# Kernel optimization log

Measured on AMD Instinct MI355X. Metric: run time of the kernel, lower is better.

The kernel has to match this reference:

```python
import jax
jax.config.update("jax_enable_x64", True)  # Sinkhorn runs in f64, matching torch's d.double()
import jax.numpy as jnp
import numpy as np

N, D, K = 32768, 128, 1024
TAU = 0.2
SK_EPS = 0.005
SK_ITERS = 3


def setup_inputs() -> dict:
    key = jax.random.key(0)
    k1, k2 = jax.random.split(key)
    x = jax.random.normal(k1, (N, D), dtype=jnp.float32)
    codebook = jax.random.normal(k2, (K, D), dtype=jnp.float32) * 0.02  # embedding.weight
    return {"x": x, "codebook": codebook}


def _l2norm(v):
    # F.normalize with eps=1e-12
    n = jnp.linalg.norm(v, axis=-1, keepdims=True)
    return v / jnp.maximum(n, 1e-12)


def _center_distance(d):
    d = jnp.where(jnp.isnan(d), jnp.zeros_like(d), d)
    mx, mn = d.max(), d.min()
    middle = (mx + mn) / 2
    amplitude = jnp.maximum(mx - middle + 1e-5, 1e-5)
    return (d - middle) / amplitude


def _sinkhorn(d, epsilon, iters):
    # d: [N, K] in f64; Q: [K, N]
    Q = jnp.exp(-d / epsilon).T
    Kc, B = Q.shape
    Q = Q / jnp.maximum(Q.sum(), 1e-5)

    def body(Q, _):
        Q = Q / Q.sum(axis=1, keepdims=True) / Kc
        Q = Q / Q.sum(axis=0, keepdims=True) / B
        return Q, None

    Q, _ = jax.lax.scan(body, Q, None, length=iters)
    return (Q * B).T  # [N, K]


def reference(x, codebook):
    latent = x.reshape(-1, codebook.shape[-1])  # [N, D]
    cos_sim = _l2norm(latent) @ _l2norm(codebook).T  # [N, K]
    d = (1.0 - cos_sim) / TAU

    # training path with sk_epsilon > 0: center + Sinkhorn (no_grad in torch)
    dc = _center_distance(jax.lax.stop_gradient(d))
    Q = _sinkhorn(dc.astype(jnp.float64), SK_EPS, SK_ITERS)
    indices = jnp.argmax(Q, axis=-1)  # [N]

    x_q = codebook[indices].reshape(x.shape)

    # cross-entropy(cos_sim / tau, indices.detach())
    logits = cos_sim / TAU
    logp = jax.nn.log_softmax(logits, axis=-1)
    loss = -jnp.mean(jnp.take_along_axis(logp, indices[:, None], axis=-1))

    # straight-through estimator
    x_q = x + jax.lax.stop_gradient(x_q - x)
    return x_q, loss, indices
```

## Files before the change

kernel.cpp:

```cpp
#include <hip/hip_runtime.h>
#include <cstddef>

#define NPTS 32768
#define DDIM 128
#define KCB  1024

typedef __attribute__((ext_vector_type(8))) short short8;
typedef __attribute__((ext_vector_type(4))) float f32x4;


__device__ __forceinline__ float hw_exp2(float x) {
#if __has_builtin(__builtin_amdgcn_exp2f)
  return __builtin_amdgcn_exp2f(x);
#else
  return exp2f(x);
#endif
}

__device__ __forceinline__ void atomic_add_f64(double* p, double v) {
  __hip_atomic_fetch_add(p, v, __ATOMIC_RELAXED, __HIP_MEMORY_SCOPE_AGENT);
}

__device__ __forceinline__ unsigned short bf16_rne(float v) {
  unsigned u = __float_as_uint(v);
  unsigned r = u + 0x7FFFu + ((u >> 16) & 1u);
  return (unsigned short)(r >> 16);
}
__device__ __forceinline__ float bf16_tof(unsigned short h) {
  return __uint_as_float((unsigned)h << 16);
}

__device__ __forceinline__ float div_mark(float x, float c, float rc) {
  float q0 = x * rc;
  float r  = fmaf(-c, q0, x);
  return fmaf(r, rc, q0);
}

__device__ __forceinline__ double sweep_E(float cv, float middle, float amp, float rc_amp) {
  float d  = div_mark(1.0f - cv, 0.2f, 1.0f / 0.2f);
  float dc = div_mark(d - middle, amp, rc_amp);
  double xl2 = (double)dc * (-288.53900817779268);
  double kd  = rint(xl2);
  float  fr  = (float)(xl2 - kd);
  float  m   = hw_exp2(fr);
  long long bits = ((long long)(1023 + (int)kd)) << 52;
  return (double)m * __longlong_as_double(bits);
}

__device__ __forceinline__ double score_exponent(float cv, float middle, float amplitude) {
  float d  = (1.0f - cv) / 0.2f;
  float dc = (d - middle) / amplitude;
  return (double)dc * (-(1.0 / 0.005));
}

__device__ __forceinline__ unsigned enc_f32(float f) {
  unsigned u = __float_as_uint(f);
  return (u & 0x80000000u) ? ~u : (u | 0x80000000u);
}
__device__ __forceinline__ float dec_f32(unsigned e) {
  unsigned u = (e & 0x80000000u) ? (e & 0x7FFFFFFFu) : ~e;
  return __uint_as_float(u);
}

#if __has_builtin(__builtin_amdgcn_global_load_lds)
#define HAVE_ASYNC_LDS 1
typedef __attribute__((address_space(3))) unsigned int lds_u32_t;
typedef const __attribute__((address_space(1))) unsigned int glb_u32_t;
__device__ __forceinline__ void async_ld16(const void* g, void* l) {
  __builtin_amdgcn_global_load_lds((glb_u32_t*)g, (lds_u32_t*)l, 16, 0, 0);
}
#else
#define HAVE_ASYNC_LDS 0
#endif


__global__ __launch_bounds__(1024) void vq_init_kernel(double* __restrict__ u123,
                                                       double* __restrict__ loss_part,
                                                       unsigned* __restrict__ maxenc,
                                                       unsigned* __restrict__ minenc) {
  int t = threadIdx.x;
  for (int i = t; i < 3 * KCB; i += 1024) u123[i] = 0.0;
  loss_part[t] = 0.0;
  if (t == 0) {
    *maxenc = 0u;
    *minenc = 0xFFFFFFFFu;
  }
}

__global__ __launch_bounds__(128) void vq_normalize_rows(const float* __restrict__ in,
                                                         float* __restrict__ out) {
  int row = blockIdx.x;
  int t = threadIdx.x;
  float v = in[(size_t)row * DDIM + t];
  float s = v * v;
#pragma unroll
  for (int off = 32; off; off >>= 1) s += __shfl_down(s, off, 64);
  __shared__ float red[2];
  if ((t & 63) == 0) red[t >> 6] = s;
  __syncthreads();
  float norm = sqrtf(red[0] + red[1]);
  out[(size_t)row * DDIM + t] = v / fmaxf(norm, 1e-12f);
}

__global__ __launch_bounds__(128) void vq_normalize_split(const float* __restrict__ in,
                                                          unsigned short* __restrict__ oh,
                                                          unsigned short* __restrict__ ol) {
  int row = blockIdx.x;
  int t = threadIdx.x;
  float v = in[(size_t)row * DDIM + t];
  float s = v * v;
#pragma unroll
  for (int off = 32; off; off >>= 1) s += __shfl_down(s, off, 64);
  __shared__ float red[2];
  if ((t & 63) == 0) red[t >> 6] = s;
  __syncthreads();
  float norm = sqrtf(red[0] + red[1]);
  float xnv = v / fmaxf(norm, 1e-12f);
  unsigned short h = bf16_rne(xnv);
  float fh = bf16_tof(h);
  unsigned short l = bf16_rne(xnv - fh);
  size_t idx = (size_t)row * DDIM + t;
  oh[idx] = h;
  ol[idx] = l;
}

#define LROWS 32

__global__ __launch_bounds__(256) void vq_gemm_mfma(const unsigned short* __restrict__ Ah,
                                                    const unsigned short* __restrict__ Al,
                                                    const unsigned short* __restrict__ Bh,
                                                    const unsigned short* __restrict__ Bl,
                                                    float* __restrict__ Cm,
                                                    unsigned* __restrict__ maxenc,
                                                    unsigned* __restrict__ minenc) {
  __shared__ unsigned short Ahs[2][128 * LROWS], Als[2][128 * LROWS];
  __shared__ unsigned short Bhs[2][128 * LROWS], Bls[2][128 * LROWS];
  __shared__ float redmx[4], redmn[4];
  int tid = threadIdx.x;
  int lane = tid & 63, wv = tid >> 6;
  int wr = wv >> 1, wc = wv & 1;
  int n0 = blockIdx.x * 128;
  int c0 = blockIdx.y * 128;
  int fr = lane & 15;
  int kq = (lane >> 4) * 8;
  f32x4 acc[4][4] = {};

  auto stage = [&](int ks, int b) {
    int kc = ks * 32;
#pragma unroll
    for (int l = 0; l < 2; ++l) {
      int idx = tid + l * 256;
      int row = idx >> 2;
      int sub = idx & 3;
      size_t ga = (size_t)(n0 + row) * DDIM + kc + sub * 8;
      size_t gb = (size_t)(c0 + row) * DDIM + kc + sub * 8;
#if HAVE_ASYNC_LDS
      int wbase = (l * 256 + wv * 64) * 8;
      async_ld16(Ah + ga, &Ahs[b][wbase]);
      async_ld16(Al + ga, &Als[b][wbase]);
      async_ld16(Bh + gb, &Bhs[b][wbase]);
      async_ld16(Bl + gb, &Bls[b][wbase]);
#else
      int lo = idx * 8;
      *(short8*)&Ahs[b][lo] = *(const short8*)(Ah + ga);
      *(short8*)&Als[b][lo] = *(const short8*)(Al + ga);
      *(short8*)&Bhs[b][lo] = *(const short8*)(Bh + gb);
      *(short8*)&Bls[b][lo] = *(const short8*)(Bl + gb);
#endif
    }
  };

  stage(0, 0);
  __syncthreads();

#pragma unroll
  for (int ks = 0; ks < 4; ++ks) {
    int cur = ks & 1;
    short8 ah[4], al[4], bh[4], bl[4];
#pragma unroll
    for (int rt = 0; rt < 4; ++rt) {
      int lo = (wr * 64 + rt * 16 + fr) * LROWS + kq;
      ah[rt] = *(const short8*)&Ahs[cur][lo];
      al[rt] = *(const short8*)&Als[cur][lo];
    }
#pragma unroll
    for (int ct = 0; ct < 4; ++ct) {
      int lo = (wc * 64 + ct * 16 + fr) * LROWS + kq;
      bh[ct] = *(const short8*)&Bhs[cur][lo];
      bl[ct] = *(const short8*)&Bls[cur][lo];
    }
    if (ks < 3) stage(ks + 1, cur ^ 1);
#pragma unroll
    for (int rt = 0; rt < 4; ++rt) {
#pragma unroll
      for (int ct = 0; ct < 4; ++ct) {
        acc[rt][ct] = __builtin_amdgcn_mfma_f32_16x16x32_bf16(ah[rt], bh[ct], acc[rt][ct], 0, 0, 0);
        acc[rt][ct] = __builtin_amdgcn_mfma_f32_16x16x32_bf16(ah[rt], bl[ct], acc[rt][ct], 0, 0, 0);
        acc[rt][ct] = __builtin_amdgcn_mfma_f32_16x16x32_bf16(al[rt], bh[ct], acc[rt][ct], 0, 0, 0);
        acc[rt][ct] = __builtin_amdgcn_mfma_f32_16x16x32_bf16(al[rt], bl[ct], acc[rt][ct], 0, 0, 0);
      }
    }
    __syncthreads();
  }

  float mx = -3.402823466e38f, mn = 3.402823466e38f;
  int orow = (lane >> 4) * 4, ocol = lane & 15;
  int rn0 = n0 + wr * 64, rc0 = c0 + wc * 64;
#pragma unroll
  for (int rt = 0; rt < 4; ++rt) {
#pragma unroll
    for (int ct = 0; ct < 4; ++ct) {
#pragma unroll
      for (int r = 0; r < 4; ++r) {
        float v = acc[rt][ct][r];
        mx = fmaxf(mx, v);
        mn = fminf(mn, v);
        Cm[(size_t)(rn0 + rt * 16 + orow + r) * KCB + (rc0 + ct * 16 + ocol)] = v;
      }
    }
  }
#pragma unroll
  for (int off = 32; off; off >>= 1) {
    mx = fmaxf(mx, __shfl_down(mx, off, 64));
    mn = fminf(mn, __shfl_down(mn, off, 64));
  }
  if (lane == 0) { redmx[wv] = mx; redmn[wv] = mn; }
  __syncthreads();
  if (tid == 0) {
    mx = fmaxf(fmaxf(redmx[0], redmx[1]), fmaxf(redmx[2], redmx[3]));
    mn = fminf(fminf(redmn[0], redmn[1]), fminf(redmn[2], redmn[3]));
    atomicMax(maxenc, enc_f32(mx));
    atomicMin(minenc, enc_f32(mn));
  }
}

__global__ void vq_scalarize(const unsigned* __restrict__ maxenc,
                             const unsigned* __restrict__ minenc,
                             float* __restrict__ scal) {
  float cosmax = dec_f32(*maxenc);
  float cosmin = dec_f32(*minenc);
  float mx_d = (1.0f - cosmin) / 0.2f;
  float mn_d = (1.0f - cosmax) / 0.2f;
  float middle = (mx_d + mn_d) / 2.0f;
  float amplitude = fmaxf(mx_d - middle + 1e-5f, 1e-5f);
  scal[0] = middle;
  scal[1] = amplitude;
  scal[2] = 1.0f / amplitude;
}

#define SROWS 32
#define SRPW  8

__global__ __launch_bounds__(256) void vq_sweep(const float* __restrict__ Cm,
                                                const float* __restrict__ scal,
                                                const double* __restrict__ Rvec,
                                                const double* __restrict__ alpha_p,
                                                double* __restrict__ u_out) {
  int t = threadIdx.x;
  int lane = t & 63, wv = t >> 6;
  int n0 = blockIdx.x * SROWS + wv * SRPW;
  float middle = scal[0], amp = scal[1], rc = scal[2];
  bool hasR = (Rvec != nullptr);
  double Rreg[16];
  double ainv = 0.0;
  if (hasR) {
#pragma unroll
    for (int c = 0; c < 4; ++c)
#pragma unroll
      for (int e = 0; e < 4; ++e) Rreg[c * 4 + e] = Rvec[c * 256 + lane * 4 + e];
    ainv = alpha_p[0] * 32768.0;
  }
  double up[16] = {};
  float4 cva[4], cvb[4];
  {
    const float4* row0 = (const float4*)(Cm + (size_t)n0 * KCB);
#pragma unroll
    for (int c = 0; c < 4; ++c) cva[c] = row0[c * 64 + lane];
  }
#pragma unroll 1
  for (int r = 0; r < SRPW; ++r) {
    int rn = (r < SRPW - 1) ? r + 1 : r;
    const float4* rown = (const float4*)(Cm + (size_t)(n0 + rn) * KCB);
#pragma unroll
    for (int c = 0; c < 4; ++c) cvb[c] = rown[c * 64 + lane];
    double e[16];
#pragma unroll
    for (int c = 0; c < 4; ++c) {
      e[c * 4 + 0] = sweep_E(cva[c].x, middle, amp, rc);
      e[c * 4 + 1] = sweep_E(cva[c].y, middle, amp, rc);
      e[c * 4 + 2] = sweep_E(cva[c].z, middle, amp, rc);
      e[c * 4 + 3] = sweep_E(cva[c].w, middle, amp, rc);
    }
    if (hasR) {
      double s = 0.0;
#pragma unroll
      for (int i = 0; i < 16; ++i) s += e[i] * Rreg[i];
#pragma unroll
      for (int off = 1; off < 64; off <<= 1) s += __shfl_xor(s, off, 64);
      double C = 1.0 / (ainv * s);
#pragma unroll
      for (int i = 0; i < 16; ++i) up[i] += e[i] * C;
    } else {
#pragma unroll
      for (int i = 0; i < 16; ++i) up[i] += e[i];
    }
#pragma unroll
    for (int c = 0; c < 4; ++c) cva[c] = cvb[c];
  }
  __shared__ double su[4][KCB];
#pragma unroll
  for (int c = 0; c < 4; ++c)
#pragma unroll
    for (int e = 0; e < 4; ++e) su[wv][c * 256 + lane * 4 + e] = up[c * 4 + e];
  __syncthreads();
#pragma unroll
  for (int j = 0; j < 4; ++j) {
    int k = (t + ((blockIdx.x + j) & 3) * 256) & (KCB - 1);
    double v = su[0][k] + su[1][k] + su[2][k] + su[3][k];
    atomic_add_f64(&u_out[k], v);
  }
}

__global__ __launch_bounds__(1024) void vq_finalize_u(const double* __restrict__ u,
                                                      double* __restrict__ alpha_p,
                                                      double* __restrict__ R,
                                                      double* __restrict__ lnR,
                                                      int mode) {
  int k = threadIdx.x;
  double uk = u[k];
  __shared__ double red[16];
  __shared__ double s_alpha;
  if (mode == 0) {
    double s = uk;
#pragma unroll
    for (int off = 32; off; off >>= 1) s += __shfl_down(s, off, 64);
    if ((k & 63) == 0) red[k >> 6] = s;
    __syncthreads();
    if (k == 0) {
      double s0 = 0.0;
      for (int w = 0; w < 16; ++w) s0 += red[w];
      double a = 1.0 / fmax(s0, 1e-5);
      s_alpha = a;
      alpha_p[0] = a;
    }
    __syncthreads();
  }
  double alpha = (mode == 0) ? s_alpha : alpha_p[0];
  double r = 1.0 / (alpha * 1024.0 * uk);
  R[k] = r;
  if (mode == 2) lnR[k] = log(r);
}

#define FRPW 4
#define MARGIN 0.08f
#define LOG2E 1.44269504088896340736f

__global__ __launch_bounds__(256) void vq_final_pass(const float* __restrict__ Cm,
                                                     const float* __restrict__ x,
                                                     const float* __restrict__ cb,
                                                     const float* __restrict__ xn,
                                                     const float* __restrict__ cn,
                                                     const double* __restrict__ lnR,
                                                     const float* __restrict__ scal,
                                                     double* __restrict__ loss_part,
                                                     float* __restrict__ out_xq,
                                                     float* __restrict__ out_idx) {
  int t = threadIdx.x;
  int lane = t & 63, wv = t >> 6;
  int n0 = blockIdx.x * (4 * FRPW) + wv * FRPW;
  float middle = scal[0], amplitude = scal[1], rc_amp = scal[2];
  float lnRf[16];
  double lnRd[16];
#pragma unroll
  for (int c = 0; c < 4; ++c)
#pragma unroll
    for (int e = 0; e < 4; ++e) {
      double v = lnR[c * 256 + lane * 4 + e];
      lnRd[c * 4 + e] = v;
      lnRf[c * 4 + e] = (float)v;
    }

  double loss_loc = 0.0;
  float4 cva[4], cvb[4];
  {
    const float4* row0 = (const float4*)(Cm + (size_t)n0 * KCB);
#pragma unroll
    for (int c = 0; c < 4; ++c) cva[c] = row0[c * 64 + lane];
  }
#pragma unroll 1
  for (int r = 0; r < FRPW; ++r) {
    int n = n0 + r;
    int rn = (r < FRPW - 1) ? r + 1 : r;
    const float4* rown = (const float4*)(Cm + (size_t)(n0 + rn) * KCB);
#pragma unroll
    for (int c = 0; c < 4; ++c) cvb[c] = rown[c * 64 + lane];

    float lv[16];
    float sv[16];
    float b1 = -3.402823466e38f, b2 = -3.402823466e38f;
    int k1 = 0;
    float lmax = -3.402823466e38f;
#pragma unroll
    for (int c = 0; c < 4; ++c) {
#pragma unroll
      for (int e = 0; e < 4; ++e) {
        float cvv = (e == 0) ? cva[c].x : (e == 1) ? cva[c].y : (e == 2) ? cva[c].z : cva[c].w;
        int k = c * 256 + lane * 4 + e;
        float d  = div_mark(1.0f - cvv, 0.2f, 5.0f);
        float dc = div_mark(d - middle, amplitude, rc_amp);
        float s  = fmaf(dc, -200.0f, lnRf[c * 4 + e]);
        sv[c * 4 + e] = s;
        if (s > b1) { b2 = b1; b1 = s; k1 = k; }
        else if (s > b2) b2 = s;
        float l = div_mark(cvv, 0.2f, 5.0f);
        lv[c * 4 + e] = l;
        lmax = fmaxf(lmax, l);
      }
    }
#pragma unroll
    for (int off = 1; off < 64; off <<= 1) {
      float o1 = __shfl_xor(b1, off, 64);
      int ok = __shfl_xor(k1, off, 64);
      float o2 = __shfl_xor(b2, off, 64);
      float om = __shfl_xor(lmax, off, 64);
      float cand2;
      if (o1 > b1 || (o1 == b1 && ok < k1)) { cand2 = fmaxf(b1, o2); b1 = o1; k1 = ok; }
      else cand2 = fmaxf(o1, o2);
      b2 = fmaxf(b2, cand2);
      lmax = fmaxf(lmax, om);
    }
    int bestk = k1;
    if (b1 - b2 < MARGIN) {
      double pbest = -1.0e308;
      int pk = KCB;
      const float* xr = xn + (size_t)n * DDIM;
      float thr = b1 - MARGIN;
#pragma unroll 1
      for (int i = 0; i < 16; ++i) {
        if (sv[i] >= thr) {
          int k = (i >> 2) * 256 + lane * 4 + (i & 3);
          const float* cr = cn + (size_t)k * DDIM;
          float dot = 0.0f;
          for (int d = 0; d < DDIM; ++d) dot = fmaf(xr[d], cr[d], dot);
          double ps = score_exponent(dot, middle, amplitude) + lnRd[i];
          if (ps > pbest || (ps == pbest && k < pk)) { pbest = ps; pk = k; }
        }
      }
#pragma unroll
      for (int off = 1; off < 64; off <<= 1) {
        double ob = __shfl_xor(pbest, off, 64);
        int ok = __shfl_xor(pk, off, 64);
        if (ob > pbest || (ob == pbest && ok < pk)) { pbest = ob; pk = ok; }
      }
      bestk = pk;
    }
    float se = 0.0f;
    float lb = 0.0f;
#pragma unroll
    for (int c = 0; c < 4; ++c) {
#pragma unroll
      for (int e = 0; e < 4; ++e) {
        int k = c * 256 + lane * 4 + e;
        se += hw_exp2((lv[c * 4 + e] - lmax) * LOG2E);
        if (k == bestk) lb = lv[c * 4 + e];
      }
    }
#pragma unroll
    for (int off = 1; off < 64; off <<= 1) {
      se += __shfl_xor(se, off, 64);
      lb += __shfl_xor(lb, off, 64);
    }
    loss_loc += (double)(-(lb - lmax - logf(se)));
    if (lane == 0) out_idx[n] = (float)bestk;
    float2 xv = *(const float2*)&x[(size_t)n * DDIM + lane * 2];
    float2 cbv = *(const float2*)&cb[(size_t)bestk * DDIM + lane * 2];
    float2 o;
    o.x = xv.x + (cbv.x - xv.x);
    o.y = xv.y + (cbv.y - xv.y);
    *(float2*)&out_xq[(size_t)n * DDIM + lane * 2] = o;
#pragma unroll
    for (int c = 0; c < 4; ++c) cva[c] = cvb[c];
  }
  if (lane == 0) atomic_add_f64(&loss_part[(blockIdx.x * 4 + wv) & (KCB - 1)], loss_loc);
}

__global__ __launch_bounds__(1024) void vq_loss_div(const double* __restrict__ lp,
                                                    float* __restrict__ out_loss) {
  int t = threadIdx.x;
  double s = lp[t];
#pragma unroll
  for (int off = 32; off; off >>= 1) s += __shfl_down(s, off, 64);
  __shared__ double red[16];
  if ((t & 63) == 0) red[t >> 6] = s;
  __syncthreads();
  if (t == 0) {
    double tot = 0.0;
    for (int w = 0; w < 16; ++w) tot += red[w];
    out_loss[0] = (float)(tot / 32768.0);
  }
}


extern "C" void kernel_launch(void* const* d_in, const int* in_sizes, int n_in,
                              void* d_out, int out_size, void* d_ws, size_t ws_size,
                              hipStream_t stream) {
  const float* x  = (const float*)d_in[0];
  const float* cb = (const float*)d_in[1];
  float* out = (float*)d_out;
  float* out_xq   = out;
  float* out_loss = out + (size_t)NPTS * DDIM;
  float* out_idx  = out + (size_t)NPTS * DDIM + 1;

  char* w = (char*)d_ws;
  unsigned short* xh = (unsigned short*)w;
  unsigned short* xl = xh + (size_t)NPTS * DDIM;
  unsigned short* ch = xl + (size_t)NPTS * DDIM;
  unsigned short* cl = ch + (size_t)KCB * DDIM;
  float* xn = (float*)w;
  float* cn = xn + (size_t)NPTS * DDIM;
  float* cosm = (float*)(w + (size_t)16896 * 1024);
  double* u1  = (double*)(cosm + (size_t)NPTS * KCB);
  double* u2  = u1 + KCB;
  double* u3  = u2 + KCB;
  double* R   = u3 + KCB;
  double* lnR = R + KCB;
  double* loss_part = lnR + KCB;
  double* alpha_p   = loss_part + KCB;
  unsigned* maxenc = (unsigned*)(alpha_p + 1);
  unsigned* minenc = maxenc + 1;
  float* scal = (float*)(minenc + 1);

  vq_init_kernel<<<1, 1024, 0, stream>>>(u1, loss_part, maxenc, minenc);

  vq_normalize_split<<<NPTS, 128, 0, stream>>>(x, xh, xl);
  vq_normalize_split<<<KCB, 128, 0, stream>>>(cb, ch, cl);
  vq_gemm_mfma<<<dim3(NPTS / 128, KCB / 128), 256, 0, stream>>>(xh, xl, ch, cl, cosm,
                                                                maxenc, minenc);

  vq_normalize_rows<<<NPTS, 128, 0, stream>>>(x, xn);
  vq_normalize_rows<<<KCB, 128, 0, stream>>>(cb, cn);
  vq_scalarize<<<1, 1, 0, stream>>>(maxenc, minenc, scal);

  vq_sweep<<<NPTS / SROWS, 256, 0, stream>>>(cosm, scal, nullptr, alpha_p, u1);
  vq_finalize_u<<<1, 1024, 0, stream>>>(u1, alpha_p, R, lnR, 0);
  vq_sweep<<<NPTS / SROWS, 256, 0, stream>>>(cosm, scal, R, alpha_p, u2);
  vq_finalize_u<<<1, 1024, 0, stream>>>(u2, alpha_p, R, lnR, 1);
  vq_sweep<<<NPTS / SROWS, 256, 0, stream>>>(cosm, scal, R, alpha_p, u3);
  vq_finalize_u<<<1, 1024, 0, stream>>>(u3, alpha_p, R, lnR, 2);

  vq_final_pass<<<NPTS / (4 * FRPW), 256, 0, stream>>>(cosm, x, cb, xn, cn, lnR, scal,
                                                       loss_part, out_xq, out_idx);
  vq_loss_div<<<1, 1024, 0, stream>>>(loss_part, out_loss);
}
```

Baseline: 317.7 us.

## Load GEMM fragments directly from global, drop LDS staging and scalarize kernel

The GEMM kernel stops staging A/B tiles through double-buffered LDS and instead loads MFMA fragments straight from global memory into registers. This removes the barriers and LDS traffic, and launch_bounds(256,2) is added. The grid is reordered so the codebook tile index varies fastest, which should improve L2 reuse of the x tiles. The tiny scalarize kernel is removed, and the sweep and final kernels now compute middle and amplitude inline from the encoded max/min. The cost is redundant global loads across waves, since rows are shared by two waves, and those loads are less coalesced 16-byte strided accesses.

New measurement: 355.1 us. +11.7%, slower.

```diff
diff --git a/kernel.cpp b/kernel.cpp
--- a/kernel.cpp
+++ b/kernel.cpp
@@ -62,16 +62,16 @@
   return __uint_as_float(u);
 }
 
-#if __has_builtin(__builtin_amdgcn_global_load_lds)
-#define HAVE_ASYNC_LDS 1
-typedef __attribute__((address_space(3))) unsigned int lds_u32_t;
-typedef const __attribute__((address_space(1))) unsigned int glb_u32_t;
-__device__ __forceinline__ void async_ld16(const void* g, void* l) {
-  __builtin_amdgcn_global_load_lds((glb_u32_t*)g, (lds_u32_t*)l, 16, 0, 0);
-}
-#else
-#define HAVE_ASYNC_LDS 0
-#endif
+__device__ __forceinline__ void calc_scal(const unsigned* maxenc, const unsigned* minenc,
+                                          float& middle, float& amplitude, float& rc_amp) {
+  float cosmax = dec_f32(*maxenc);
+  float cosmin = dec_f32(*minenc);
+  float mx_d = (1.0f - cosmin) / 0.2f;
+  float mn_d = (1.0f - cosmax) / 0.2f;
+  middle = (mx_d + mn_d) / 2.0f;
+  amplitude = fmaxf(mx_d - middle + 1e-5f, 1e-5f);
+  rc_amp = 1.0f / amplitude;
+}
 
 
 __global__ __launch_bounds__(1024) void vq_init_kernel(double* __restrict__ u123,
@@ -124,72 +124,42 @@
   ol[idx] = l;
 }
 
-#define LROWS 32
-
-__global__ __launch_bounds__(256) void vq_gemm_mfma(const unsigned short* __restrict__ Ah,
-                                                    const unsigned short* __restrict__ Al,
-                                                    const unsigned short* __restrict__ Bh,
-                                                    const unsigned short* __restrict__ Bl,
-                                                    float* __restrict__ Cm,
-                                                    unsigned* __restrict__ maxenc,
-                                                    unsigned* __restrict__ minenc) {
-  __shared__ unsigned short Ahs[2][128 * LROWS], Als[2][128 * LROWS];
-  __shared__ unsigned short Bhs[2][128 * LROWS], Bls[2][128 * LROWS];
+
+__global__ __launch_bounds__(256, 2) void vq_gemm_mfma(const unsigned short* __restrict__ Ah,
+                                                       const unsigned short* __restrict__ Al,
+                                                       const unsigned short* __restrict__ Bh,
+                                                       const unsigned short* __restrict__ Bl,
+                                                       float* __restrict__ Cm,
+                                                       unsigned* __restrict__ maxenc,
+                                                       unsigned* __restrict__ minenc) {
   __shared__ float redmx[4], redmn[4];
   int tid = threadIdx.x;
   int lane = tid & 63, wv = tid >> 6;
   int wr = wv >> 1, wc = wv & 1;
-  int n0 = blockIdx.x * 128;
-  int c0 = blockIdx.y * 128;
+  int c0 = blockIdx.x * 128;
+  int n0 = blockIdx.y * 128;
   int fr = lane & 15;
   int kq = (lane >> 4) * 8;
   f32x4 acc[4][4] = {};
 
-  auto stage = [&](int ks, int b) {
-    int kc = ks * 32;
-#pragma unroll
-    for (int l = 0; l < 2; ++l) {
-      int idx = tid + l * 256;
-      int row = idx >> 2;
-      int sub = idx & 3;
-      size_t ga = (size_t)(n0 + row) * DDIM + kc + sub * 8;
-      size_t gb = (size_t)(c0 + row) * DDIM + kc + sub * 8;
-#if HAVE_ASYNC_LDS
-      int wbase = (l * 256 + wv * 64) * 8;
-      async_ld16(Ah + ga, &Ahs[b][wbase]);
-      async_ld16(Al + ga, &Als[b][wbase]);
-      async_ld16(Bh + gb, &Bhs[b][wbase]);
-      async_ld16(Bl + gb, &Bls[b][wbase]);
-#else
-      int lo = idx * 8;
-      *(short8*)&Ahs[b][lo] = *(const short8*)(Ah + ga);
-      *(short8*)&Als[b][lo] = *(const short8*)(Al + ga);
-      *(short8*)&Bhs[b][lo] = *(const short8*)(Bh + gb);
-      *(short8*)&Bls[b][lo] = *(const short8*)(Bl + gb);
-#endif
-    }
-  };
-
-  stage(0, 0);
-  __syncthreads();
+  size_t aoff[4], boff[4];
+#pragma unroll
+  for (int rt = 0; rt < 4; ++rt)
+    aoff[rt] = (size_t)(n0 + wr * 64 + rt * 16 + fr) * DDIM + kq;
+#pragma unroll
+  for (int ct = 0; ct < 4; ++ct)
+    boff[ct] = (size_t)(c0 + wc * 64 + ct * 16 + fr) * DDIM + kq;
 
 #pragma unroll
   for (int ks = 0; ks < 4; ++ks) {
-    int cur = ks & 1;
     short8 ah[4], al[4], bh[4], bl[4];
 #pragma unroll
-    for (int rt = 0; rt < 4; ++rt) {
-      int lo = (wr * 64 + rt * 16 + fr) * LROWS + kq;
-      ah[rt] = *(const short8*)&Ahs[cur][lo];
-      al[rt] = *(const short8*)&Als[cur][lo];
-    }
-#pragma unroll
-    for (int ct = 0; ct < 4; ++ct) {
-      int lo = (wc * 64 + ct * 16 + fr) * LROWS + kq;
-      bh[ct] = *(const short8*)&Bhs[cur][lo];
-      bl[ct] = *(const short8*)&Bls[cur][lo];
-    }
-    if (ks < 3) stage(ks + 1, cur ^ 1);
+    for (int i = 0; i < 4; ++i) {
+      ah[i] = *(const short8*)(Ah + aoff[i] + ks * 32);
+      al[i] = *(const short8*)(Al + aoff[i] + ks * 32);
+      bh[i] = *(const short8*)(Bh + boff[i] + ks * 32);
+      bl[i] = *(const short8*)(Bl + boff[i] + ks * 32);
+    }
 #pragma unroll
     for (int rt = 0; rt < 4; ++rt) {
 #pragma unroll
@@ -200,7 +170,6 @@
         acc[rt][ct] = __builtin_amdgcn_mfma_f32_16x16x32_bf16(al[rt], bl[ct], acc[rt][ct], 0, 0, 0);
       }
     }
-    __syncthreads();
   }
 
   float mx = -3.402823466e38f, mn = 3.402823466e38f;
@@ -234,32 +203,20 @@
   }
 }
 
-__global__ void vq_scalarize(const unsigned* __restrict__ maxenc,
-                             const unsigned* __restrict__ minenc,
-                             float* __restrict__ scal) {
-  float cosmax = dec_f32(*maxenc);
-  float cosmin = dec_f32(*minenc);
-  float mx_d = (1.0f - cosmin) / 0.2f;
-  float mn_d = (1.0f - cosmax) / 0.2f;
-  float middle = (mx_d + mn_d) / 2.0f;
-  float amplitude = fmaxf(mx_d - middle + 1e-5f, 1e-5f);
-  scal[0] = middle;
-  scal[1] = amplitude;
-  scal[2] = 1.0f / amplitude;
-}
-
 #define SROWS 32
 #define SRPW  8
 
 __global__ __launch_bounds__(256) void vq_sweep(const float* __restrict__ Cm,
-                                                const float* __restrict__ scal,
+                                                const unsigned* __restrict__ maxenc,
+                                                const unsigned* __restrict__ minenc,
                                                 const double* __restrict__ Rvec,
                                                 const double* __restrict__ alpha_p,
                                                 double* __restrict__ u_out) {
   int t = threadIdx.x;
   int lane = t & 63, wv = t >> 6;
   int n0 = blockIdx.x * SROWS + wv * SRPW;
-  float middle = scal[0], amp = scal[1], rc = scal[2];
+  float middle, amp, rc;
+  calc_scal(maxenc, minenc, middle, amp, rc);
   bool hasR = (Rvec != nullptr);
   double Rreg[16];
   double ainv = 0.0;
@@ -361,14 +318,16 @@
                                                      const float* __restrict__ xn,
                                                      const float* __restrict__ cn,
                                                      const double* __restrict__ lnR,
-                                                     const float* __restrict__ scal,
+                                                     const unsigned* __restrict__ maxenc,
+                                                     const unsigned* __restrict__ minenc,
                                                      double* __restrict__ loss_part,
                                                      float* __restrict__ out_xq,
                                                      float* __restrict__ out_idx) {
   int t = threadIdx.x;
   int lane = t & 63, wv = t >> 6;
   int n0 = blockIdx.x * (4 * FRPW) + wv * FRPW;
-  float middle = scal[0], amplitude = scal[1], rc_amp = scal[2];
+  float middle, amplitude, rc_amp;
+  calc_scal(maxenc, minenc, middle, amplitude, rc_amp);
   float lnRf[16];
   double lnRd[16];
 #pragma unroll
@@ -528,27 +487,26 @@
   double* alpha_p   = loss_part + KCB;
   unsigned* maxenc = (unsigned*)(alpha_p + 1);
   unsigned* minenc = maxenc + 1;
-  float* scal = (float*)(minenc + 1);
 
   vq_init_kernel<<<1, 1024, 0, stream>>>(u1, loss_part, maxenc, minenc);
 
   vq_normalize_split<<<NPTS, 128, 0, stream>>>(x, xh, xl);
   vq_normalize_split<<<KCB, 128, 0, stream>>>(cb, ch, cl);
-  vq_gemm_mfma<<<dim3(NPTS / 128, KCB / 128), 256, 0, stream>>>(xh, xl, ch, cl, cosm,
+  vq_gemm_mfma<<<dim3(KCB / 128, NPTS / 128), 256, 0, stream>>>(xh, xl, ch, cl, cosm,
                                                                 maxenc, minenc);
 
   vq_normalize_rows<<<NPTS, 128, 0, stream>>>(x, xn);
   vq_normalize_rows<<<KCB, 128, 0, stream>>>(cb, cn);
-  vq_scalarize<<<1, 1, 0, stream>>>(maxenc, minenc, scal);
-
-  vq_sweep<<<NPTS / SROWS, 256, 0, stream>>>(cosm, scal, nullptr, alpha_p, u1);
+
+  vq_sweep<<<NPTS / SROWS, 256, 0, stream>>>(cosm, maxenc, minenc, nullptr, alpha_p, u1);
   vq_finalize_u<<<1, 1024, 0, stream>>>(u1, alpha_p, R, lnR, 0);
-  vq_sweep<<<NPTS / SROWS, 256, 0, stream>>>(cosm, scal, R, alpha_p, u2);
+  vq_sweep<<<NPTS / SROWS, 256, 0, stream>>>(cosm, maxenc, minenc, R, alpha_p, u2);
   vq_finalize_u<<<1, 1024, 0, stream>>>(u2, alpha_p, R, lnR, 1);
-  vq_sweep<<<NPTS / SROWS, 256, 0, stream>>>(cosm, scal, R, alpha_p, u3);
+  vq_sweep<<<NPTS / SROWS, 256, 0, stream>>>(cosm, maxenc, minenc, R, alpha_p, u3);
   vq_finalize_u<<<1, 1024, 0, stream>>>(u3, alpha_p, R, lnR, 2);
 
-  vq_final_pass<<<NPTS / (4 * FRPW), 256, 0, stream>>>(cosm, x, cb, xn, cn, lnR, scal,
+  vq_final_pass<<<NPTS / (4 * FRPW), 256, 0, stream>>>(cosm, x, cb, xn, cn, lnR,
+                                                       maxenc, minenc,
                                                        loss_part, out_xq, out_idx);
   vq_loss_div<<<1, 1024, 0, stream>>>(loss_part, out_loss);
 }
```
